# Optimization experiments

Measured on AMD Instinct MI355X. Metric: run time of the kernel, lower is better.

## Reference

```python
import jax, jax.numpy as jnp
import numpy as np

CH = 512
GROUPS = 8
EPS = 1e-5


def setup_inputs() -> dict:
    key = jax.random.key(0)
    ks = jax.random.split(key, 5)
    B, C, H, W = 16, CH, 32, 32
    x = jax.random.normal(ks[0], (B, C, H, W), dtype=jnp.float32)
    # GroupNorm affine params
    norm_w = jnp.ones((C,), dtype=jnp.float32)
    norm_b = jnp.zeros((C,), dtype=jnp.float32)
    # 1x1 conv == linear over channels; store weights as [out, in]
    qkv_w = jax.random.normal(ks[1], (3 * C, C), dtype=jnp.float32) * (C ** -0.5)
    qkv_b = jnp.zeros((3 * C,), dtype=jnp.float32)
    proj_w = jax.random.normal(ks[2], (C, C), dtype=jnp.float32) * (C ** -0.5)
    proj_b = jnp.zeros((C,), dtype=jnp.float32)
    return {"x": x, "norm_w": norm_w, "norm_b": norm_b,
            "qkv_w": qkv_w, "qkv_b": qkv_b,
            "proj_w": proj_w, "proj_b": proj_b}


def _group_norm(x, w, b):
    B, C, H, W = x.shape
    g = GROUPS
    xg = x.reshape(B, g, C // g, H * W)
    mean = xg.mean(axis=(2, 3), keepdims=True)
    var = xg.var(axis=(2, 3), keepdims=True)
    xn = (xg - mean) * jax.lax.rsqrt(var + EPS)
    xn = xn.reshape(B, C, H, W)
    return xn * w[None, :, None, None] + b[None, :, None, None]


def reference(x, norm_w, norm_b, qkv_w, qkv_b, proj_w, proj_b):
    B, C, H, W = x.shape
    h = _group_norm(x, norm_w, norm_b)  # [B,C,H,W]
    hs = h.reshape(B, C, H * W)  # spatial tokens along last axis
    # 1x1 conv QKV: [3C,C] @ [B,C,N] -> [B,3C,N]
    qkv = jnp.einsum('oc,bcn->bon', qkv_w, hs) + qkv_b[None, :, None]
    q, k, v = jnp.split(qkv, 3, axis=1)  # each [B,C,N]
    scale = C ** (-0.5)
    attn = jnp.einsum('bci,bcj->bij', q, k) * scale  # [B,N,N]
    attn = jax.nn.softmax(attn, axis=-1)
    out = jnp.einsum('bij,bcj->bci', attn, v)  # [B,C,N]
    out = jnp.einsum('oc,bcn->bon', proj_w, out) + proj_b[None, :, None]
    return x + out.reshape(B, C, H, W)
```

## Files before the change

### kernel.cpp

```cpp
#include <hip/hip_runtime.h>
#include <math.h>

#define Bn  16
#define Cn  512
#define Nn  1024
#define Gn  8
#define CPG 64
#define EPSf 1e-5f

typedef short           bf16x8 __attribute__((ext_vector_type(8)));
typedef float           f32x4  __attribute__((ext_vector_type(4)));
typedef unsigned short  u16;
typedef unsigned short  u16x4  __attribute__((ext_vector_type(4)));
typedef unsigned short  u16x8  __attribute__((ext_vector_type(8)));

__device__ __forceinline__ u16 f2b(float f) {
  union { float f; unsigned u; } c; c.f = f;
  unsigned r = (c.u + 0x7FFFu + ((c.u >> 16) & 1u)) >> 16;
  return (u16)r;
}

__device__ __forceinline__ void g2l16(const void* g, void* l) {
  __builtin_amdgcn_global_load_lds(
      (const __attribute__((address_space(1))) unsigned int*)g,
      (__attribute__((address_space(3))) unsigned int*)l, 16, 0, 0);
}

__global__ __launch_bounds__(256) void prep_k(const float* __restrict__ qkv_w,
    const float* __restrict__ proj_w, const float* __restrict__ x,
    u16* __restrict__ wq16, u16* __restrict__ wp16, float* __restrict__ stats) {
  int blk = blockIdx.x, t = threadIdx.x;
  if (blk < 1024) {
    const float* src = (blk < 768) ? qkv_w : proj_w;
    u16* dst = (blk < 768) ? wq16 : wp16;
    int i = (blk < 768 ? blk : blk - 768) * 256 + t;
    float4 v = ((const float4*)src)[i];
    u16x4 o;
    o.x = f2b(v.x); o.y = f2b(v.y); o.z = f2b(v.z); o.w = f2b(v.w);
    ((u16x4*)dst)[i] = o;
    return;
  }
  int bg = blk - 1024;
  const float4* xp = (const float4*)(x + (size_t)bg * (CPG * Nn));
  float s = 0.f, ss = 0.f;
  const int cnt4 = CPG * Nn / 4;
  for (int i = t; i < cnt4; i += 256) {
    float4 v = xp[i];
    s  += v.x + v.y + v.z + v.w;
    ss += v.x*v.x + v.y*v.y + v.z*v.z + v.w*v.w;
  }
  #pragma unroll
  for (int off = 32; off > 0; off >>= 1) {
    s  += __shfl_down(s, off);
    ss += __shfl_down(ss, off);
  }
  __shared__ float sm[4], sq[4];
  int lane = t & 63, wid = t >> 6;
  if (lane == 0) { sm[wid] = s; sq[wid] = ss; }
  __syncthreads();
  if (t == 0) {
    float S  = sm[0] + sm[1] + sm[2] + sm[3];
    float SS = sq[0] + sq[1] + sq[2] + sq[3];
    const float inv = 1.0f / (float)(CPG * Nn);
    float m = S * inv;
    float var = SS * inv - m * m;
    stats[bg]       = m;
    stats[128 + bg] = rsqrtf(var + EPSf);
  }
}

__global__ __launch_bounds__(256) void gn_apply_t_k(const float* __restrict__ x,
    const float* __restrict__ stats, const float* __restrict__ nw,
    const float* __restrict__ nb, u16* __restrict__ hT) {
  int b = blockIdx.z, c0 = blockIdx.y * 64, n0 = blockIdx.x * 64;
  __shared__ u16 T[64][68];
  int t = threadIdx.x;
  int row = t >> 4, col4 = t & 15;
  #pragma unroll
  for (int it = 0; it < 4; it++) {
    int cc = row + it * 16;
    int c  = c0 + cc;
    int bg = b * Gn + (c >> 6);
    float mean = stats[bg], rs = stats[128 + bg];
    float a  = nw[c] * rs;
    float bb = nb[c] - mean * a;
    float4 xv = *(const float4*)&x[((size_t)(b * Cn + c)) * Nn + n0 + col4 * 4];
    u16x4 o;
    o.x = f2b(xv.x * a + bb); o.y = f2b(xv.y * a + bb);
    o.z = f2b(xv.z * a + bb); o.w = f2b(xv.w * a + bb);
    *(u16x4*)&T[cc][col4 * 4] = o;
  }
  __syncthreads();
  #pragma unroll
  for (int it = 0; it < 2; it++) {
    int ch = t + it * 256;
    int n  = ch >> 3, c8 = (ch & 7) * 8;
    u16x8 o;
    #pragma unroll
    for (int j = 0; j < 8; j++) o[j] = T[c8 + j][n];
    *(u16x8*)&hT[((size_t)(b * Nn + n0 + n)) * Cn + c0 + c8] = o;
  }
}

__device__ __forceinline__ void gemm_core(const u16* __restrict__ A, size_t sA,
                                          const u16* __restrict__ B, size_t sB,
                                          int K, f32x4 acc[4][4]) {
  __shared__ u16 As[128 * 32];
  __shared__ u16 Bs[128 * 32];
  const int t = threadIdx.x;
  const int w = t >> 6, l = t & 63, quad = l >> 4, lr = l & 15;
  const int wm = (w >> 1) * 64, wn = (w & 1) * 64;

  const int ra = w * 16 + (l >> 2);
  const int p  = l & 3;
  const int q  = p ^ ((ra >> 1) & 3);
  const u16* gA0 = A + (size_t)ra * sA + q * 8;
  const u16* gA1 = A + (size_t)(ra + 64) * sA + q * 8;
  const u16* gB0 = B + (size_t)ra * sB + q * 8;
  const u16* gB1 = B + (size_t)(ra + 64) * sB + q * 8;
  u16* lA0 = As + ra * 32 + p * 8;
  u16* lA1 = As + (ra + 64) * 32 + p * 8;
  u16* lB0 = Bs + ra * 32 + p * 8;
  u16* lB1 = Bs + (ra + 64) * 32 + p * 8;

  for (int k0 = 0; k0 < K; k0 += 32) {
    __syncthreads();
    g2l16(gA0 + k0, lA0);
    g2l16(gA1 + k0, lA1);
    g2l16(gB0 + k0, lB0);
    g2l16(gB1 + k0, lB1);
    __syncthreads();
    bf16x8 af[4], bfr[4];
    #pragma unroll
    for (int fm = 0; fm < 4; fm++) {
      int r = wm + fm * 16 + lr;
      af[fm] = *(const bf16x8*)&As[r * 32 + ((quad ^ ((r >> 1) & 3)) << 3)];
    }
    #pragma unroll
    for (int fn = 0; fn < 4; fn++) {
      int r = wn + fn * 16 + lr;
      bfr[fn] = *(const bf16x8*)&Bs[r * 32 + ((quad ^ ((r >> 1) & 3)) << 3)];
    }
    #pragma unroll
    for (int fm = 0; fm < 4; fm++)
      #pragma unroll
      for (int fn = 0; fn < 4; fn++)
        acc[fm][fn] = __builtin_amdgcn_mfma_f32_16x16x32_bf16(
            af[fm], bfr[fn], acc[fm][fn], 0, 0, 0);
  }
}

#define GEMM_PRE()                                              \
  const int t = threadIdx.x;                                    \
  const int w = t >> 6, l = t & 63, quad = l >> 4, lr = l & 15; \
  const int wm = (w >> 1) * 64, wn = (w & 1) * 64;              \
  f32x4 acc[4][4];                                              \
  { f32x4 z = {0.f, 0.f, 0.f, 0.f};                             \
    for (int i = 0; i < 4; i++)                                 \
      for (int j = 0; j < 4; j++) acc[i][j] = z; }

__global__ __launch_bounds__(256) void gemm_qkv_k(const u16* __restrict__ w16,
    const u16* __restrict__ hT, const float* __restrict__ bias,
    u16* __restrict__ qkT, u16* __restrict__ v) {
  int b = blockIdx.z, m0 = blockIdx.y * 128, n0 = blockIdx.x * 128;
  GEMM_PRE();
  gemm_core(w16 + (size_t)m0 * Cn, Cn,
            hT + ((size_t)b * Nn + n0) * Cn, Cn, Cn, acc);
  #pragma unroll
  for (int fm = 0; fm < 4; fm++) {
    int mb = m0 + wm + fm * 16 + quad * 4;
    float b0 = bias[mb], b1 = bias[mb + 1], b2 = bias[mb + 2], b3 = bias[mb + 3];
    #pragma unroll
    for (int fn = 0; fn < 4; fn++) {
      int n = n0 + wn + fn * 16 + lr;
      f32x4 a = acc[fm][fn];
      if (m0 < 1024) {
        u16x4 o;
        o.x = f2b(a[0] + b0); o.y = f2b(a[1] + b1);
        o.z = f2b(a[2] + b2); o.w = f2b(a[3] + b3);
        *(u16x4*)&qkT[((size_t)(b * Nn + n)) * 1024 + mb] = o;
      } else {
        int c = mb - 1024;
        v[((size_t)(b * Cn + c    )) * Nn + n] = f2b(a[0] + b0);
        v[((size_t)(b * Cn + c + 1)) * Nn + n] = f2b(a[1] + b1);
        v[((size_t)(b * Cn + c + 2)) * Nn + n] = f2b(a[2] + b2);
        v[((size_t)(b * Cn + c + 3)) * Nn + n] = f2b(a[3] + b3);
      }
    }
  }
}

__global__ __launch_bounds__(256) void gemm_qk_k(const u16* __restrict__ qkT,
    u16* __restrict__ P, float* __restrict__ rpart) {
  int b = blockIdx.z, i0 = blockIdx.y * 128, j0 = blockIdx.x * 128;
  const u16* base = qkT + (size_t)b * Nn * 1024;
  __shared__ float psum[128];
  GEMM_PRE();
  gemm_core(base + (size_t)i0 * 1024, 1024,
            base + (size_t)j0 * 1024 + 512, 1024, Cn, acc);
  if (t < 128) psum[t] = 0.f;
  __syncthreads();
  const float scale = 0.04419417382415922f;
  #pragma unroll
  for (int fm = 0; fm < 4; fm++) {
    int ri = wm + fm * 16 + quad * 4;
    float rs0 = 0.f, rs1 = 0.f, rs2 = 0.f, rs3 = 0.f;
    #pragma unroll
    for (int fn = 0; fn < 4; fn++) {
      int j = j0 + wn + fn * 16 + lr;
      f32x4 a = acc[fm][fn];
      float p0 = __expf(a[0] * scale);
      float p1 = __expf(a[1] * scale);
      float p2 = __expf(a[2] * scale);
      float p3 = __expf(a[3] * scale);
      u16* Pp = &P[((size_t)(b * Nn + i0 + ri)) * Nn + j];
      Pp[0]              = f2b(p0);
      Pp[Nn]             = f2b(p1);
      Pp[2 * Nn]         = f2b(p2);
      Pp[3 * (size_t)Nn] = f2b(p3);
      rs0 += p0; rs1 += p1; rs2 += p2; rs3 += p3;
    }
    #pragma unroll
    for (int mask = 1; mask < 16; mask <<= 1) {
      rs0 += __shfl_xor(rs0, mask);
      rs1 += __shfl_xor(rs1, mask);
      rs2 += __shfl_xor(rs2, mask);
      rs3 += __shfl_xor(rs3, mask);
    }
    if (lr == 0) {
      atomicAdd(&psum[ri],     rs0);
      atomicAdd(&psum[ri + 1], rs1);
      atomicAdd(&psum[ri + 2], rs2);
      atomicAdd(&psum[ri + 3], rs3);
    }
  }
  __syncthreads();
  if (t < 128)
    rpart[((size_t)(b * 8) + blockIdx.x) * Nn + i0 + t] = psum[t];
}

__global__ __launch_bounds__(256) void gemm_pv_k(const u16* __restrict__ P,
    const u16* __restrict__ v, const float* __restrict__ rpart,
    u16* __restrict__ O) {
  int b = blockIdx.z, i0 = blockIdx.y * 128, c0 = blockIdx.x * 128;
  __shared__ float rinv[128];
  {
    int t0 = threadIdx.x;
    if (t0 < 128) {
      float s = 0.f;
      #pragma unroll
      for (int jb = 0; jb < 8; jb++)
        s += rpart[((size_t)(b * 8 + jb)) * Nn + i0 + t0];
      rinv[t0] = 1.0f / s;
    }
  }
  GEMM_PRE();
  gemm_core(P + ((size_t)b * Nn + i0) * Nn, Nn,
            v + ((size_t)b * Cn + c0) * Nn, Nn, Nn, acc);
  #pragma unroll
  for (int fm = 0; fm < 4; fm++) {
    int ri = wm + fm * 16 + quad * 4;
    int ib = i0 + ri;
    #pragma unroll
    for (int fn = 0; fn < 4; fn++) {
      int c = c0 + wn + fn * 16 + lr;
      f32x4 a = acc[fm][fn];
      O[((size_t)(b * Nn + ib    )) * Cn + c] = f2b(a[0] * rinv[ri]);
      O[((size_t)(b * Nn + ib + 1)) * Cn + c] = f2b(a[1] * rinv[ri + 1]);
      O[((size_t)(b * Nn + ib + 2)) * Cn + c] = f2b(a[2] * rinv[ri + 2]);
      O[((size_t)(b * Nn + ib + 3)) * Cn + c] = f2b(a[3] * rinv[ri + 3]);
    }
  }
}

__global__ __launch_bounds__(256) void gemm_proj_k(const u16* __restrict__ pw16,
    const u16* __restrict__ O, const float* __restrict__ bias,
    const float* __restrict__ x, float* __restrict__ out) {
  int b = blockIdx.z, m0 = blockIdx.y * 128, n0 = blockIdx.x * 128;
  GEMM_PRE();
  gemm_core(pw16 + (size_t)m0 * Cn, Cn,
            O + ((size_t)b * Nn + n0) * Cn, Cn, Cn, acc);
  #pragma unroll
  for (int fm = 0; fm < 4; fm++) {
    int mb = m0 + wm + fm * 16 + quad * 4;
    #pragma unroll
    for (int fn = 0; fn < 4; fn++) {
      int n = n0 + wn + fn * 16 + lr;
      f32x4 a = acc[fm][fn];
      #pragma unroll
      for (int r = 0; r < 4; r++) {
        size_t oi = ((size_t)(b * Cn + mb + r)) * Nn + n;
        out[oi] = a[r] + bias[mb + r] + x[oi];
      }
    }
  }
}

extern "C" void kernel_launch(void* const* d_in, const int* in_sizes, int n_in,
                              void* d_out, int out_size, void* d_ws, size_t ws_size,
                              hipStream_t stream) {
  const float* x      = (const float*)d_in[0];
  const float* norm_w = (const float*)d_in[1];
  const float* norm_b = (const float*)d_in[2];
  const float* qkv_w  = (const float*)d_in[3];
  const float* qkv_b  = (const float*)d_in[4];
  const float* proj_w = (const float*)d_in[5];
  const float* proj_b = (const float*)d_in[6];
  float* out = (float*)d_out;
  char* ws = (char*)d_ws;

  u16*   wq16  = (u16*)(ws);
  u16*   wp16  = (u16*)(ws + 1572864);
  u16*   hT    = (u16*)(ws + 2097152);
  u16*   qkT   = (u16*)(ws + 35651584);
  u16*   v     = (u16*)(ws + 69206016);
  u16*   P     = (u16*)(ws + 85983232);
  u16*   O     = (u16*)(ws + 119537664);
  float* stats = (float*)(ws + 136314880);
  float* rpart = (float*)(ws + 136315904);

  prep_k<<<1152, 256, 0, stream>>>(qkv_w, proj_w, x, wq16, wp16, stats);
  gn_apply_t_k<<<dim3(Nn / 64, Cn / 64, Bn), 256, 0, stream>>>(x, stats, norm_w, norm_b, hT);
  gemm_qkv_k<<<dim3(Nn / 128, 1536 / 128, Bn), 256, 0, stream>>>(wq16, hT, qkv_b, qkT, v);
  gemm_qk_k<<<dim3(Nn / 128, Nn / 128, Bn), 256, 0, stream>>>(qkT, P, rpart);
  gemm_pv_k<<<dim3(Cn / 128, Nn / 128, Bn), 256, 0, stream>>>(P, v, rpart, O);
  gemm_proj_k<<<dim3(Nn / 128, Cn / 128, Bn), 256, 0, stream>>>(wp16, O, proj_b, x, out);
}
```

Measured before the change: 254.7 us.

## Fold projection weight into V to remove separate proj GEMM

Precomputes W2 = proj_w · Wv (plus a folded bias), so the value path produces proj_w·V directly. The PV GEMM then writes the final output with normalization, bias and residual in its epilogue, which removes the separate projection GEMM and the O intermediate buffer. Kernels are also merged (weight prep with stats, W2 GEMM with the GroupNorm apply) to cut launches. The trade-off is an extra small weight GEMM each call and a different bf16 rounding order.

Measured after the change: 242.5 us. 1.05x faster.

```diff
diff --git a/kernel.cpp b/kernel.cpp
--- a/kernel.cpp
+++ b/kernel.cpp
@@ -1,11 +1,11 @@
 #include <hip/hip_runtime.h>
 #include <math.h>
 
-#define Bn  16
-#define Cn  512
-#define Nn  1024
-#define Gn  8
-#define CPG 64
+#define Bn   16
+#define Cn   512
+#define Nn   1024
+#define Gn   8
+#define CPG  64
 #define EPSf 1e-5f
 
 typedef short           bf16x8 __attribute__((ext_vector_type(8)));
@@ -26,87 +26,9 @@
       (__attribute__((address_space(3))) unsigned int*)l, 16, 0, 0);
 }
 
-__global__ __launch_bounds__(256) void prep_k(const float* __restrict__ qkv_w,
-    const float* __restrict__ proj_w, const float* __restrict__ x,
-    u16* __restrict__ wq16, u16* __restrict__ wp16, float* __restrict__ stats) {
-  int blk = blockIdx.x, t = threadIdx.x;
-  if (blk < 1024) {
-    const float* src = (blk < 768) ? qkv_w : proj_w;
-    u16* dst = (blk < 768) ? wq16 : wp16;
-    int i = (blk < 768 ? blk : blk - 768) * 256 + t;
-    float4 v = ((const float4*)src)[i];
-    u16x4 o;
-    o.x = f2b(v.x); o.y = f2b(v.y); o.z = f2b(v.z); o.w = f2b(v.w);
-    ((u16x4*)dst)[i] = o;
-    return;
-  }
-  int bg = blk - 1024;
-  const float4* xp = (const float4*)(x + (size_t)bg * (CPG * Nn));
-  float s = 0.f, ss = 0.f;
-  const int cnt4 = CPG * Nn / 4;
-  for (int i = t; i < cnt4; i += 256) {
-    float4 v = xp[i];
-    s  += v.x + v.y + v.z + v.w;
-    ss += v.x*v.x + v.y*v.y + v.z*v.z + v.w*v.w;
-  }
-  #pragma unroll
-  for (int off = 32; off > 0; off >>= 1) {
-    s  += __shfl_down(s, off);
-    ss += __shfl_down(ss, off);
-  }
-  __shared__ float sm[4], sq[4];
-  int lane = t & 63, wid = t >> 6;
-  if (lane == 0) { sm[wid] = s; sq[wid] = ss; }
-  __syncthreads();
-  if (t == 0) {
-    float S  = sm[0] + sm[1] + sm[2] + sm[3];
-    float SS = sq[0] + sq[1] + sq[2] + sq[3];
-    const float inv = 1.0f / (float)(CPG * Nn);
-    float m = S * inv;
-    float var = SS * inv - m * m;
-    stats[bg]       = m;
-    stats[128 + bg] = rsqrtf(var + EPSf);
-  }
-}
-
-__global__ __launch_bounds__(256) void gn_apply_t_k(const float* __restrict__ x,
-    const float* __restrict__ stats, const float* __restrict__ nw,
-    const float* __restrict__ nb, u16* __restrict__ hT) {
-  int b = blockIdx.z, c0 = blockIdx.y * 64, n0 = blockIdx.x * 64;
-  __shared__ u16 T[64][68];
-  int t = threadIdx.x;
-  int row = t >> 4, col4 = t & 15;
-  #pragma unroll
-  for (int it = 0; it < 4; it++) {
-    int cc = row + it * 16;
-    int c  = c0 + cc;
-    int bg = b * Gn + (c >> 6);
-    float mean = stats[bg], rs = stats[128 + bg];
-    float a  = nw[c] * rs;
-    float bb = nb[c] - mean * a;
-    float4 xv = *(const float4*)&x[((size_t)(b * Cn + c)) * Nn + n0 + col4 * 4];
-    u16x4 o;
-    o.x = f2b(xv.x * a + bb); o.y = f2b(xv.y * a + bb);
-    o.z = f2b(xv.z * a + bb); o.w = f2b(xv.w * a + bb);
-    *(u16x4*)&T[cc][col4 * 4] = o;
-  }
-  __syncthreads();
-  #pragma unroll
-  for (int it = 0; it < 2; it++) {
-    int ch = t + it * 256;
-    int n  = ch >> 3, c8 = (ch & 7) * 8;
-    u16x8 o;
-    #pragma unroll
-    for (int j = 0; j < 8; j++) o[j] = T[c8 + j][n];
-    *(u16x8*)&hT[((size_t)(b * Nn + n0 + n)) * Cn + c0 + c8] = o;
-  }
-}
-
-__device__ __forceinline__ void gemm_core(const u16* __restrict__ A, size_t sA,
-                                          const u16* __restrict__ B, size_t sB,
-                                          int K, f32x4 acc[4][4]) {
-  __shared__ u16 As[128 * 32];
-  __shared__ u16 Bs[128 * 32];
+__device__ __forceinline__ void gemm_core(u16* As, u16* Bs,
+    const u16* __restrict__ A, size_t sA,
+    const u16* __restrict__ B, size_t sB, int K, f32x4 acc[4][4]) {
   const int t = threadIdx.x;
   const int w = t >> 6, l = t & 63, quad = l >> 4, lr = l & 15;
   const int wm = (w >> 1) * 64, wn = (w & 1) * 64;
@@ -154,50 +76,202 @@
   const int t = threadIdx.x;                                    \
   const int w = t >> 6, l = t & 63, quad = l >> 4, lr = l & 15; \
   const int wm = (w >> 1) * 64, wn = (w & 1) * 64;              \
+  (void)w; (void)wm; (void)wn;                                  \
   f32x4 acc[4][4];                                              \
   { f32x4 z = {0.f, 0.f, 0.f, 0.f};                             \
-    for (int i = 0; i < 4; i++)                                 \
-      for (int j = 0; j < 4; j++) acc[i][j] = z; }
-
-__global__ __launch_bounds__(256) void gemm_qkv_k(const u16* __restrict__ w16,
-    const u16* __restrict__ hT, const float* __restrict__ bias,
-    u16* __restrict__ qkT, u16* __restrict__ v) {
-  int b = blockIdx.z, m0 = blockIdx.y * 128, n0 = blockIdx.x * 128;
+    for (int i_ = 0; i_ < 4; i_++)                              \
+      for (int j_ = 0; j_ < 4; j_++) acc[i_][j_] = z; }
+
+__global__ __launch_bounds__(256) void prep_k(const float* __restrict__ qkv_w,
+    const float* __restrict__ proj_w, const float* __restrict__ qkv_b,
+    const float* __restrict__ x, u16* __restrict__ wqk16,
+    u16* __restrict__ wvT16, u16* __restrict__ pw16,
+    float* __restrict__ bias2, float* __restrict__ stats) {
+  __shared__ u16 T[64][68];
+  __shared__ float sm[4], sq[4];
+  int bid = blockIdx.x, t = threadIdx.x;
+  if (bid < 512) {
+    int i = bid * 256 + t;
+    float4 v = ((const float4*)qkv_w)[i];
+    u16x4 o;
+    o.x = f2b(v.x); o.y = f2b(v.y); o.z = f2b(v.z); o.w = f2b(v.w);
+    ((u16x4*)wqk16)[i] = o;
+  } else if (bid < 576) {
+    int tile = bid - 512, tx = tile & 7, ty = tile >> 3;
+    int row = t >> 4, col4 = t & 15;
+    #pragma unroll
+    for (int it = 0; it < 4; it++) {
+      int cc = row + it * 16;
+      float4 v = *(const float4*)&qkv_w[(size_t)(1024 + ty * 64 + cc) * 512 + tx * 64 + col4 * 4];
+      u16x4 o;
+      o.x = f2b(v.x); o.y = f2b(v.y); o.z = f2b(v.z); o.w = f2b(v.w);
+      *(u16x4*)&T[cc][col4 * 4] = o;
+    }
+    __syncthreads();
+    #pragma unroll
+    for (int it = 0; it < 2; it++) {
+      int ch = t + it * 256;
+      int d = ch >> 3, c8 = (ch & 7) * 8;
+      u16x8 o;
+      #pragma unroll
+      for (int j = 0; j < 8; j++) o[j] = T[c8 + j][d];
+      *(u16x8*)&wvT16[(size_t)(tx * 64 + d) * 512 + ty * 64 + c8] = o;
+    }
+  } else if (bid < 578) {
+    int m = (bid - 576) * 256 + t;
+    float s = 0.f;
+    for (int c = 0; c < 512; c++)
+      s += proj_w[(size_t)m * 512 + c] * qkv_b[1024 + c];
+    bias2[m] = s;
+  } else if (bid < 706) {
+    int bg = bid - 578;
+    const float4* xp = (const float4*)(x + (size_t)bg * (CPG * Nn));
+    float s = 0.f, ss = 0.f;
+    const int cnt4 = CPG * Nn / 4;
+    for (int i = t; i < cnt4; i += 256) {
+      float4 v = xp[i];
+      s  += v.x + v.y + v.z + v.w;
+      ss += v.x * v.x + v.y * v.y + v.z * v.z + v.w * v.w;
+    }
+    #pragma unroll
+    for (int off = 32; off > 0; off >>= 1) {
+      s  += __shfl_down(s, off);
+      ss += __shfl_down(ss, off);
+    }
+    int lane = t & 63, wid = t >> 6;
+    if (lane == 0) { sm[wid] = s; sq[wid] = ss; }
+    __syncthreads();
+    if (t == 0) {
+      float S  = sm[0] + sm[1] + sm[2] + sm[3];
+      float SS = sq[0] + sq[1] + sq[2] + sq[3];
+      const float inv = 1.0f / (float)(CPG * Nn);
+      float m = S * inv;
+      float var = SS * inv - m * m;
+      stats[bg]       = m;
+      stats[128 + bg] = rsqrtf(var + EPSf);
+    }
+  } else {
+    int i = (bid - 706) * 256 + t;
+    float4 v = ((const float4*)proj_w)[i];
+    u16x4 o;
+    o.x = f2b(v.x); o.y = f2b(v.y); o.z = f2b(v.z); o.w = f2b(v.w);
+    ((u16x4*)pw16)[i] = o;
+  }
+}
+
+__global__ __launch_bounds__(256) void gnw2_k(const float* __restrict__ x,
+    const float* __restrict__ stats, const float* __restrict__ nw,
+    const float* __restrict__ nb, const u16* __restrict__ pw16,
+    const u16* __restrict__ wvT16, u16* __restrict__ W2, u16* __restrict__ hT) {
+  __shared__ u16 AsBs[8192];
+  int bid = blockIdx.x;
+  if (bid < 16) {
+    int m0 = (bid >> 2) * 128, d0 = (bid & 3) * 128;
+    GEMM_PRE();
+    gemm_core(AsBs, AsBs + 4096, pw16 + (size_t)m0 * 512, 512,
+              wvT16 + (size_t)d0 * 512, 512, 512, acc);
+    #pragma unroll
+    for (int fm = 0; fm < 4; fm++) {
+      int m = m0 + wm + fm * 16 + quad * 4;
+      #pragma unroll
+      for (int fn = 0; fn < 4; fn++) {
+        int d = d0 + wn + fn * 16 + lr;
+        f32x4 a = acc[fm][fn];
+        W2[(size_t)(m    ) * 512 + d] = f2b(a[0]);
+        W2[(size_t)(m + 1) * 512 + d] = f2b(a[1]);
+        W2[(size_t)(m + 2) * 512 + d] = f2b(a[2]);
+        W2[(size_t)(m + 3) * 512 + d] = f2b(a[3]);
+      }
+    }
+    return;
+  }
+  int u = bid - 16;
+  int b = u >> 7, rem = u & 127, c0 = (rem >> 4) * 64, n0 = (rem & 15) * 64;
+  u16 (*T)[68] = (u16(*)[68])AsBs;
+  int t = threadIdx.x;
+  int row = t >> 4, col4 = t & 15;
+  #pragma unroll
+  for (int it = 0; it < 4; it++) {
+    int cc = row + it * 16;
+    int c  = c0 + cc;
+    int bg = b * Gn + (c >> 6);
+    float mean = stats[bg], rstd = stats[128 + bg];
+    float a  = nw[c] * rstd;
+    float bb = nb[c] - mean * a;
+    float4 xv = *(const float4*)&x[((size_t)(b * Cn + c)) * Nn + n0 + col4 * 4];
+    u16x4 o;
+    o.x = f2b(xv.x * a + bb); o.y = f2b(xv.y * a + bb);
+    o.z = f2b(xv.z * a + bb); o.w = f2b(xv.w * a + bb);
+    *(u16x4*)&T[cc][col4 * 4] = o;
+  }
+  __syncthreads();
+  #pragma unroll
+  for (int it = 0; it < 2; it++) {
+    int ch = t + it * 256;
+    int n  = ch >> 3, c8 = (ch & 7) * 8;
+    u16x8 o;
+    #pragma unroll
+    for (int j = 0; j < 8; j++) o[j] = T[c8 + j][n];
+    *(u16x8*)&hT[((size_t)(b * Nn + n0 + n)) * 512 + c0 + c8] = o;
+  }
+}
+
+__global__ __launch_bounds__(256) void qkvp_k(const u16* __restrict__ wqk16,
+    const u16* __restrict__ W2, const u16* __restrict__ hT,
+    const float* __restrict__ qkv_b, u16* __restrict__ qkT,
+    u16* __restrict__ VP) {
+  __shared__ u16 AsBs[8192];
+  int u = blockIdx.x;
   GEMM_PRE();
-  gemm_core(w16 + (size_t)m0 * Cn, Cn,
-            hT + ((size_t)b * Nn + n0) * Cn, Cn, Cn, acc);
-  #pragma unroll
-  for (int fm = 0; fm < 4; fm++) {
-    int mb = m0 + wm + fm * 16 + quad * 4;
-    float b0 = bias[mb], b1 = bias[mb + 1], b2 = bias[mb + 2], b3 = bias[mb + 3];
-    #pragma unroll
-    for (int fn = 0; fn < 4; fn++) {
-      int n = n0 + wn + fn * 16 + lr;
-      f32x4 a = acc[fm][fn];
-      if (m0 < 1024) {
+  if (u < 1024) {
+    int b = u >> 6, rem = u & 63, m0 = (rem >> 3) * 128, n0 = (rem & 7) * 128;
+    gemm_core(AsBs, AsBs + 4096, wqk16 + (size_t)m0 * 512, 512,
+              hT + ((size_t)(b * Nn + n0)) * 512, 512, 512, acc);
+    #pragma unroll
+    for (int fm = 0; fm < 4; fm++) {
+      int mb = m0 + wm + fm * 16 + quad * 4;
+      float b0 = qkv_b[mb], b1 = qkv_b[mb + 1], b2 = qkv_b[mb + 2], b3 = qkv_b[mb + 3];
+      #pragma unroll
+      for (int fn = 0; fn < 4; fn++) {
+        int n = n0 + wn + fn * 16 + lr;
+        f32x4 a = acc[fm][fn];
         u16x4 o;
         o.x = f2b(a[0] + b0); o.y = f2b(a[1] + b1);
         o.z = f2b(a[2] + b2); o.w = f2b(a[3] + b3);
         *(u16x4*)&qkT[((size_t)(b * Nn + n)) * 1024 + mb] = o;
-      } else {
-        int c = mb - 1024;
-        v[((size_t)(b * Cn + c    )) * Nn + n] = f2b(a[0] + b0);
-        v[((size_t)(b * Cn + c + 1)) * Nn + n] = f2b(a[1] + b1);
-        v[((size_t)(b * Cn + c + 2)) * Nn + n] = f2b(a[2] + b2);
-        v[((size_t)(b * Cn + c + 3)) * Nn + n] = f2b(a[3] + b3);
       }
     }
-  }
-}
-
-__global__ __launch_bounds__(256) void gemm_qk_k(const u16* __restrict__ qkT,
-    u16* __restrict__ P, float* __restrict__ rpart) {
-  int b = blockIdx.z, i0 = blockIdx.y * 128, j0 = blockIdx.x * 128;
+  } else {
+    int u2 = u - 1024;
+    int b = u2 >> 5, rem = u2 & 31, m0 = (rem >> 3) * 128, j0 = (rem & 7) * 128;
+    gemm_core(AsBs, AsBs + 4096, W2 + (size_t)m0 * 512, 512,
+              hT + ((size_t)(b * Nn + j0)) * 512, 512, 512, acc);
+    #pragma unroll
+    for (int fm = 0; fm < 4; fm++) {
+      int m = m0 + wm + fm * 16 + quad * 4;
+      #pragma unroll
+      for (int fn = 0; fn < 4; fn++) {
+        int j = j0 + wn + fn * 16 + lr;
+        f32x4 a = acc[fm][fn];
+        VP[((size_t)(b * 512 + m    )) * 1024 + j] = f2b(a[0]);
+        VP[((size_t)(b * 512 + m + 1)) * 1024 + j] = f2b(a[1]);
+        VP[((size_t)(b * 512 + m + 2)) * 1024 + j] = f2b(a[2]);
+        VP[((size_t)(b * 512 + m + 3)) * 1024 + j] = f2b(a[3]);
+      }
+    }
+  }
+}
+
+__global__ __launch_bounds__(256) void qkexp_k(const u16* __restrict__ qkT,
+    u16* __restrict__ Pm, float* __restrict__ rpart) {
+  __shared__ u16 AsBs[8192];
+  __shared__ float psum[128];
+  int u = blockIdx.x;
+  int b = u >> 6, rem = u & 63, i0 = (rem >> 3) * 128, j0 = (rem & 7) * 128;
   const u16* base = qkT + (size_t)b * Nn * 1024;
-  __shared__ float psum[128];
   GEMM_PRE();
-  gemm_core(base + (size_t)i0 * 1024, 1024,
-            base + (size_t)j0 * 1024 + 512, 1024, Cn, acc);
+  gemm_core(AsBs, AsBs + 4096, base + (size_t)i0 * 1024, 1024,
+            base + (size_t)j0 * 1024 + 512, 1024, 512, acc);
   if (t < 128) psum[t] = 0.f;
   __syncthreads();
   const float scale = 0.04419417382415922f;
@@ -213,11 +287,11 @@
       float p1 = __expf(a[1] * scale);
       float p2 = __expf(a[2] * scale);
       float p3 = __expf(a[3] * scale);
-      u16* Pp = &P[((size_t)(b * Nn + i0 + ri)) * Nn + j];
-      Pp[0]              = f2b(p0);
-      Pp[Nn]             = f2b(p1);
-      Pp[2 * Nn]         = f2b(p2);
-      Pp[3 * (size_t)Nn] = f2b(p3);
+      u16* Pp = &Pm[((size_t)(b * Nn + i0 + ri)) * 1024 + j];
+      Pp[0]    = f2b(p0);
+      Pp[1024] = f2b(p1);
+      Pp[2048] = f2b(p2);
+      Pp[3072] = f2b(p3);
       rs0 += p0; rs1 += p1; rs2 += p2; rs3 += p3;
     }
     #pragma unroll
@@ -236,62 +310,45 @@
   }
   __syncthreads();
   if (t < 128)
-    rpart[((size_t)(b * 8) + blockIdx.x) * Nn + i0 + t] = psum[t];
-}
-
-__global__ __launch_bounds__(256) void gemm_pv_k(const u16* __restrict__ P,
-    const u16* __restrict__ v, const float* __restrict__ rpart,
-    u16* __restrict__ O) {
-  int b = blockIdx.z, i0 = blockIdx.y * 128, c0 = blockIdx.x * 128;
+    rpart[((size_t)(b * 8) + (rem & 7)) * 1024 + i0 + t] = psum[t];
+}
+
+__global__ __launch_bounds__(256) void pvout_k(const u16* __restrict__ VP,
+    const u16* __restrict__ Pm, const float* __restrict__ rpart,
+    const float* __restrict__ bias2, const float* __restrict__ proj_b,
+    const float* __restrict__ x, float* __restrict__ out) {
+  __shared__ u16 AsBs[8192];
   __shared__ float rinv[128];
-  {
-    int t0 = threadIdx.x;
-    if (t0 < 128) {
-      float s = 0.f;
-      #pragma unroll
-      for (int jb = 0; jb < 8; jb++)
-        s += rpart[((size_t)(b * 8 + jb)) * Nn + i0 + t0];
-      rinv[t0] = 1.0f / s;
-    }
+  int bid = blockIdx.x;
+  int b = bid >> 5, rem = bid & 31, m0 = (rem >> 3) * 128, i0 = (rem & 7) * 128;
+  if (threadIdx.x < 128) {
+    float s = 0.f;
+    #pragma unroll
+    for (int jb = 0; jb < 8; jb++)
+      s += rpart[((size_t)(b * 8 + jb)) * 1024 + i0 + threadIdx.x];
+    rinv[threadIdx.x] = 1.0f / s;
   }
   GEMM_PRE();
-  gemm_core(P + ((size_t)b * Nn + i0) * Nn, Nn,
-            v + ((size_t)b * Cn + c0) * Nn, Nn, Nn, acc);
+  gemm_core(AsBs, AsBs + 4096, VP + ((size_t)(b * 512 + m0)) * 1024, 1024,
+            Pm + ((size_t)(b * Nn + i0)) * 1024, 1024, 1024, acc);
   #pragma unroll
   for (int fm = 0; fm < 4; fm++) {
-    int ri = wm + fm * 16 + quad * 4;
-    int ib = i0 + ri;
+    int m = m0 + wm + fm * 16 + quad * 4;
+    float c0 = bias2[m    ] + proj_b[m    ];
+    float c1 = bias2[m + 1] + proj_b[m + 1];
+    float c2 = bias2[m + 2] + proj_b[m + 2];
+    float c3 = bias2[m + 3] + proj_b[m + 3];
     #pragma unroll
     for (int fn = 0; fn < 4; fn++) {
-      int c = c0 + wn + fn * 16 + lr;
+      int il = wn + fn * 16 + lr;
+      int i  = i0 + il;
+      float ri = rinv[il];
       f32x4 a = acc[fm][fn];
-      O[((size_t)(b * Nn + ib    )) * Cn + c] = f2b(a[0] * rinv[ri]);
-      O[((size_t)(b * Nn + ib + 1)) * Cn + c] = f2b(a[1] * rinv[ri + 1]);
-      O[((size_t)(b * Nn + ib + 2)) * Cn + c] = f2b(a[2] * rinv[ri + 2]);
-      O[((size_t)(b * Nn + ib + 3)) * Cn + c] = f2b(a[3] * rinv[ri + 3]);
-    }
-  }
-}
-
-__global__ __launch_bounds__(256) void gemm_proj_k(const u16* __restrict__ pw16,
-    const u16* __restrict__ O, const float* __restrict__ bias,
-    const float* __restrict__ x, float* __restrict__ out) {
-  int b = blockIdx.z, m0 = blockIdx.y * 128, n0 = blockIdx.x * 128;
-  GEMM_PRE();
-  gemm_core(pw16 + (size_t)m0 * Cn, Cn,
-            O + ((size_t)b * Nn + n0) * Cn, Cn, Cn, acc);
-  #pragma unroll
-  for (int fm = 0; fm < 4; fm++) {
-    int mb = m0 + wm + fm * 16 + quad * 4;
-    #pragma unroll
-    for (int fn = 0; fn < 4; fn++) {
-      int n = n0 + wn + fn * 16 + lr;
-      f32x4 a = acc[fm][fn];
-      #pragma unroll
-      for (int r = 0; r < 4; r++) {
-        size_t oi = ((size_t)(b * Cn + mb + r)) * Nn + n;
-        out[oi] = a[r] + bias[mb + r] + x[oi];
-      }
+      size_t o0 = ((size_t)(b * Cn + m)) * Nn + i;
+      out[o0                  ] = a[0] * ri + c0 + x[o0                  ];
+      out[o0 + Nn             ] = a[1] * ri + c1 + x[o0 + Nn             ];
+      out[o0 + 2 * Nn         ] = a[2] * ri + c2 + x[o0 + 2 * Nn         ];
+      out[o0 + 3 * (size_t)Nn] = a[3] * ri + c3 + x[o0 + 3 * (size_t)Nn];
     }
   }
 }
@@ -309,20 +366,21 @@
   float* out = (float*)d_out;
   char* ws = (char*)d_ws;
 
-  u16*   wq16  = (u16*)(ws);
-  u16*   wp16  = (u16*)(ws + 1572864);
-  u16*   hT    = (u16*)(ws + 2097152);
-  u16*   qkT   = (u16*)(ws + 35651584);
-  u16*   v     = (u16*)(ws + 69206016);
-  u16*   P     = (u16*)(ws + 85983232);
-  u16*   O     = (u16*)(ws + 119537664);
-  float* stats = (float*)(ws + 136314880);
-  float* rpart = (float*)(ws + 136315904);
-
-  prep_k<<<1152, 256, 0, stream>>>(qkv_w, proj_w, x, wq16, wp16, stats);
-  gn_apply_t_k<<<dim3(Nn / 64, Cn / 64, Bn), 256, 0, stream>>>(x, stats, norm_w, norm_b, hT);
-  gemm_qkv_k<<<dim3(Nn / 128, 1536 / 128, Bn), 256, 0, stream>>>(wq16, hT, qkv_b, qkT, v);
-  gemm_qk_k<<<dim3(Nn / 128, Nn / 128, Bn), 256, 0, stream>>>(qkT, P, rpart);
-  gemm_pv_k<<<dim3(Cn / 128, Nn / 128, Bn), 256, 0, stream>>>(P, v, rpart, O);
-  gemm_proj_k<<<dim3(Nn / 128, Cn / 128, Bn), 256, 0, stream>>>(wp16, O, proj_b, x, out);
-}
+  u16*   wqk16 = (u16*)(ws);
+  u16*   wvT16 = (u16*)(ws + 1048576);
+  u16*   pw16  = (u16*)(ws + 1572864);
+  u16*   W2    = (u16*)(ws + 2097152);
+  float* bias2 = (float*)(ws + 2621440);
+  float* stats = (float*)(ws + 2623488);
+  u16*   hT    = (u16*)(ws + 2624512);
+  u16*   qkT   = (u16*)(ws + 19401728);
+  u16*   VP    = (u16*)(ws + 52956160);
+  u16*   Pm    = (u16*)(ws + 69733376);
+  float* rpart = (float*)(ws + 103287808);
+
+  prep_k<<<962, 256, 0, stream>>>(qkv_w, proj_w, qkv_b, x, wqk16, wvT16, pw16, bias2, stats);
+  gnw2_k<<<2064, 256, 0, stream>>>(x, stats, norm_w, norm_b, pw16, wvT16, W2, hT);
+  qkvp_k<<<1536, 256, 0, stream>>>(wqk16, W2, hT, qkv_b, qkT, VP);
+  qkexp_k<<<1024, 256, 0, stream>>>(qkT, Pm, rpart);
+  pvout_k<<<512, 256, 0, stream>>>(VP, Pm, rpart, bias2, proj_b, x, out);
+}
```
